# Kernel tuning notes

Measured on AMD Instinct MI355X. Metric: run time of the kernel, lower is better.

The kernel has to match this reference:

```python
import jax, jax.numpy as jnp
import numpy as np

B, T, E = 2, 4096, 1024
H = 16
D = E // H  # head_len = 64


def setup_inputs() -> dict:
    key = jax.random.key(0)
    ks = jax.random.split(key, 6)
    s = 1.0 / np.sqrt(E)
    return {
        "x": jax.random.normal(ks[0], (B, T, E), dtype=jnp.float32),
        # torch nn.Linear weights: shape (out, in), y = x @ W.T
        "Wq": jax.random.uniform(ks[1], (E, E), jnp.float32, -s, s),
        "Wk": jax.random.uniform(ks[2], (E, E), jnp.float32, -s, s),
        "Wv": jax.random.uniform(ks[3], (E, E), jnp.float32, -s, s),
        "Wo": jax.random.uniform(ks[4], (E, E), jnp.float32, -s, s),
        "bo": jax.random.uniform(ks[5], (E,), jnp.float32, -s, s),
    }


def reference(x, Wq, Wk, Wv, Wo, bo):
    Bx, Tx, Ex = x.shape
    q = x @ Wq.T
    k = x @ Wk.T
    v = x @ Wv.T
    # (B, T, H, D) -> (B, H, T, D)
    q = q.reshape(Bx, Tx, H, D).transpose(0, 2, 1, 3)
    k = k.reshape(Bx, Tx, H, D).transpose(0, 2, 1, 3)
    v = v.reshape(Bx, Tx, H, D).transpose(0, 2, 1, 3)
    # scores: (B, H, T, T), scaled by sqrt(head_len)
    sim = jnp.einsum("bhqd,bhkd->bhqk", q, k) / jnp.sqrt(jnp.float32(D))
    causal = jnp.tril(jnp.ones((Tx, Tx), dtype=bool))  # True = keep
    sim = jnp.where(causal[None, None], sim, -jnp.inf)
    attn = jax.nn.softmax(sim, axis=-1)
    # dropout_rate = 0.0 (eval) -> identity
    out = jnp.einsum("bhqk,bhkd->bhqd", attn, v)
    out = out.transpose(0, 2, 1, 3).reshape(Bx, Tx, Ex)
    return out @ Wo.T + bo
```

## Files before the change

kernel.cpp:

```cpp
#include <hip/hip_runtime.h>

typedef unsigned short bf16_t;
typedef __bf16 bf16x8 __attribute__((ext_vector_type(8)));
typedef float  v4f   __attribute__((ext_vector_type(4)));

__device__ __forceinline__ bf16_t f2bf(float f) {
    union { float f; unsigned u; } a; a.f = f;
    unsigned r = a.u + 0x7FFFu + ((a.u >> 16) & 1u);
    return (bf16_t)(r >> 16);
}
__device__ __forceinline__ unsigned fbits(float f) {
    union { float f; unsigned u; } a; a.f = f; return a.u;
}
__device__ __forceinline__ unsigned pk_trunc(float lo, float hi) {
    return (fbits(lo) >> 16) | (fbits(hi) & 0xFFFF0000u);
}

#define GL16(g, l) __builtin_amdgcn_global_load_lds( \
    (__attribute__((address_space(1))) void*)(g),    \
    (__attribute__((address_space(3))) void*)(l), 16, 0, 0)

#define QSCALE 0.18033688011f

__global__ __launch_bounds__(256) void cvt_all(
    const float4* __restrict__ x,  const float4* __restrict__ wq,
    const float4* __restrict__ wk, const float4* __restrict__ wv,
    const float4* __restrict__ wo,
    ushort4* __restrict__ xb, ushort4* __restrict__ wqkv, ushort4* __restrict__ wob) {
    int i = blockIdx.x * 256 + threadIdx.x;
    const float4* s; ushort4* d; int off;
    if (i < 2097152) { s = x; d = xb; off = i; }
    else {
        int wdx = (i - 2097152) >> 18;
        off = (i - 2097152) & 262143;
        if      (wdx == 0) { s = wq; d = wqkv; }
        else if (wdx == 1) { s = wk; d = wqkv + 262144; }
        else if (wdx == 2) { s = wv; d = wqkv + 524288; }
        else               { s = wo; d = wob; }
    }
    float4 v = s[off];
    ushort4 o;
    o.x = f2bf(v.x); o.y = f2bf(v.y); o.z = f2bf(v.z); o.w = f2bf(v.w);
    d[off] = o;
}

#define GEMM_MAINLOOP(A_, W_)                                                          \
    __shared__ bf16_t SMEM[8192];                                                      \
    bf16_t* As = SMEM; bf16_t* Bs = SMEM + 4096;                                       \
    const int tid = threadIdx.x;                                                       \
    const int w = tid >> 6, lane = tid & 63;                                           \
    const int lrow = lane & 15, lq = lane >> 4;                                        \
    const int m0 = blockIdx.y * 128, n0 = blockIdx.x * 128;                            \
    const int srow = w * 16 + (lane >> 2);                                             \
    const int sk = (lane & 3) * 8;                                                     \
    const int wm = (w & 1) * 64, wn = (w >> 1) * 64;                                   \
    v4f acc[4][4];                                                                     \
    _Pragma("unroll") for (int i = 0; i < 4; ++i)                                      \
        _Pragma("unroll") for (int j = 0; j < 4; ++j)                                  \
            acc[i][j] = (v4f){0.f, 0.f, 0.f, 0.f};                                     \
    for (int k0 = 0; k0 < 1024; k0 += 32) {                                            \
        __syncthreads();                                                               \
        GL16(A_ + (size_t)(m0 + srow) * 1024 + k0 + sk,      (char*)As + w * 1024);    \
        GL16(A_ + (size_t)(m0 + 64 + srow) * 1024 + k0 + sk, (char*)As + 4096 + w * 1024); \
        GL16(W_ + (size_t)(n0 + srow) * 1024 + k0 + sk,      (char*)Bs + w * 1024);    \
        GL16(W_ + (size_t)(n0 + 64 + srow) * 1024 + k0 + sk, (char*)Bs + 4096 + w * 1024); \
        __syncthreads();                                                               \
        bf16x8 af[4], bf[4];                                                           \
        _Pragma("unroll") for (int i = 0; i < 4; ++i)                                  \
            af[i] = *(const bf16x8*)&As[(wm + i * 16 + lrow) * 32 + lq * 8];           \
        _Pragma("unroll") for (int j = 0; j < 4; ++j)                                  \
            bf[j] = *(const bf16x8*)&Bs[(wn + j * 16 + lrow) * 32 + lq * 8];           \
        _Pragma("unroll") for (int i = 0; i < 4; ++i)                                  \
            _Pragma("unroll") for (int j = 0; j < 4; ++j)                              \
                acc[i][j] = __builtin_amdgcn_mfma_f32_16x16x32_bf16(af[i], bf[j],      \
                                                                    acc[i][j], 0, 0, 0); \
    }

__global__ __launch_bounds__(256) void gemm_qkv_kernel(
    const bf16_t* __restrict__ A, const bf16_t* __restrict__ W,
    bf16_t* __restrict__ Qb, bf16_t* __restrict__ Kb, bf16_t* __restrict__ Vtb) {
    GEMM_MAINLOOP(A, W)
    const int x = blockIdx.x;
    const int b = m0 >> 12, t0 = m0 & 4095;
    if (x < 8) {
#pragma unroll
        for (int i = 0; i < 4; ++i)
#pragma unroll
            for (int j = 0; j < 4; ++j)
#pragma unroll
                for (int r = 0; r < 4; ++r) {
                    int t = t0 + wm + i * 16 + lq * 4 + r;
                    int n = n0 + wn + j * 16 + lrow;
                    int h = n >> 6, d = n & 63;
                    Qb[(((size_t)b * 16 + h) * 4096 + t) * 64 + d] =
                        f2bf(acc[i][j][r] * QSCALE);
                }
    } else if (x < 16) {
#pragma unroll
        for (int i = 0; i < 4; ++i)
#pragma unroll
            for (int j = 0; j < 4; ++j)
#pragma unroll
                for (int r = 0; r < 4; ++r) {
                    int t = t0 + wm + i * 16 + lq * 4 + r;
                    int nn = n0 + wn + j * 16 + lrow - 1024;
                    int h = nn >> 6, d = nn & 63;
                    Kb[(((size_t)b * 16 + h) * 4096 + t) * 64 + d] = f2bf(acc[i][j][r]);
                }
    } else {
        const int d0 = n0 - 2048;
#pragma unroll 1
        for (int p = 0; p < 2; ++p) {
            __syncthreads();
            if ((w >> 1) == p) {
#pragma unroll
                for (int i = 0; i < 4; ++i)
#pragma unroll
                    for (int j = 0; j < 4; ++j) {
                        int row = j * 16 + lrow;
                        int swz = (row & 7) << 1;
                        int g = (wm >> 2) + i * 4 + lq;
                        uint2 u;
                        u.x = (unsigned)f2bf(acc[i][j][0]) | ((unsigned)f2bf(acc[i][j][1]) << 16);
                        u.y = (unsigned)f2bf(acc[i][j][2]) | ((unsigned)f2bf(acc[i][j][3]) << 16);
                        *(uint2*)&SMEM[row * 128 + ((g ^ swz) << 2)] = u;
                    }
            }
            __syncthreads();
#pragma unroll
            for (int uu = 0; uu < 4; ++uu) {
                int unit = tid + 256 * uu;
                int row = unit >> 4, seg = unit & 15;
                uint4 val = *(const uint4*)&SMEM[row * 128 + ((seg ^ (row & 7)) << 3)];
                *(uint4*)&Vtb[((size_t)b * 1024 + d0 + p * 64 + row) * 4096 + t0 + seg * 8] = val;
            }
        }
    }
}

__global__ __launch_bounds__(256) void gemm_out_kernel(
    const bf16_t* __restrict__ A, const bf16_t* __restrict__ W,
    const float* __restrict__ bo, float* __restrict__ out) {
    GEMM_MAINLOOP(A, W)
#pragma unroll
    for (int j = 0; j < 4; ++j) {
        int n = n0 + wn + j * 16 + lrow;
        float bias = bo[n];
#pragma unroll
        for (int i = 0; i < 4; ++i)
#pragma unroll
            for (int r = 0; r < 4; ++r) {
                int m = m0 + wm + i * 16 + lq * 4 + r;
                out[(size_t)m * 1024 + n] = acc[i][j][r] + bias;
            }
    }
}

__global__ __launch_bounds__(256, 2) void attn_kernel(
    const bf16_t* __restrict__ Q, const bf16_t* __restrict__ K,
    const bf16_t* __restrict__ Vt, bf16_t* __restrict__ O) {
    __shared__ bf16_t Kls[2][2][64 * 32];
    __shared__ bf16_t Vls[2][2][64 * 32];
    __shared__ bf16_t Plds[4][32 * 64];
    const int tid = threadIdx.x;
    const int w = tid >> 6, lane = tid & 63;
    const int lrow = lane & 15, lq = lane >> 4;
    const int bh = blockIdx.y;
    const int g = blockIdx.x;

    const bf16_t* Qh = Q + (size_t)bh * (4096 * 64);
    const bf16_t* Kh = K + (size_t)bh * (4096 * 64);
    const bf16_t* Vh = Vt + (size_t)bh * (64 * 4096);
    bf16_t* Pw = Plds[w];
    const int b = bh >> 4, h = bh & 15;

    const int srow = lane >> 2;
    const int soff = (((lane & 3) ^ (srow & 3))) * 8;
    const int kswz = (lq ^ (lrow & 3)) * 8;
    const int pswz = (lrow & 7) << 1;

    bf16x8 ones;
#pragma unroll
    for (int i = 0; i < 8; ++i) ones[i] = (__bf16)1.0f;

#pragma unroll 1
    for (int mem = 0; mem < 2; ++mem) {
        const int j = mem ? (31 - g) : g;
        const int q0 = j * 128;
        const int q0w = q0 + w * 32;
        const int nt = 2 * j + 2;
        const int wlast = 2 * j + (w >> 1);

        bf16x8 qf[2][2];
#pragma unroll
        for (int sub = 0; sub < 2; ++sub)
#pragma unroll
            for (int dk = 0; dk < 2; ++dk)
                qf[sub][dk] = *(const bf16x8*)&Qh[(size_t)(q0w + sub * 16 + lrow) * 64 + dk * 32 + lq * 8];

        v4f oacc[2][4];
        v4f lacc[2];
#pragma unroll
        for (int s2 = 0; s2 < 2; ++s2) {
            lacc[s2] = (v4f){0.f, 0.f, 0.f, 0.f};
#pragma unroll
            for (int d = 0; d < 4; ++d) oacc[s2][d] = (v4f){0.f, 0.f, 0.f, 0.f};
        }

        auto stage = [&](int kt, int buf) {
            const int kc0 = kt << 6;
#pragma unroll
            for (int i = 0; i < 2; ++i) {
                int idx = w * 2 + i;
                int half = idx >> 2, rg = idx & 3;
                GL16(Kh + (size_t)(kc0 + rg * 16 + srow) * 64 + half * 32 + soff,
                     (char*)&Kls[buf][half][rg * 512]);
                GL16(Vh + (size_t)(rg * 16 + srow) * 4096 + kc0 + half * 32 + soff,
                     (char*)&Vls[buf][half][rg * 512]);
            }
        };

        stage(0, 0);
        for (int kt = 0; kt < nt; ++kt) {
            const int buf = kt & 1;
            __syncthreads();
            if (kt + 1 < nt) stage(kt + 1, buf ^ 1);
            if (kt > wlast) continue;
            const int kc0 = kt << 6;
            const bool diag = (kt == wlast);

            bf16x8 kf0[4], kf1[4];
#pragma unroll
            for (int c = 0; c < 4; ++c) {
                kf0[c] = *(const bf16x8*)&Kls[buf][0][(c * 16 + lrow) * 32 + kswz];
                kf1[c] = *(const bf16x8*)&Kls[buf][1][(c * 16 + lrow) * 32 + kswz];
            }
            bf16x8 vf[4][2];
#pragma unroll
            for (int d = 0; d < 4; ++d)
#pragma unroll
                for (int kh = 0; kh < 2; ++kh)
                    vf[d][kh] = *(const bf16x8*)&Vls[buf][kh][(d * 16 + lrow) * 32 + kswz];

#pragma unroll
            for (int sub = 0; sub < 2; ++sub) {
                const int qrow = sub * 16 + lrow;
                const int qglob = q0w + qrow;

                v4f st[4];
#pragma unroll
                for (int c = 0; c < 4; ++c) {
                    v4f t0v = (v4f){0.f, 0.f, 0.f, 0.f};
                    t0v = __builtin_amdgcn_mfma_f32_16x16x32_bf16(kf0[c], qf[sub][0], t0v, 0, 0, 0);
                    st[c] = __builtin_amdgcn_mfma_f32_16x16x32_bf16(kf1[c], qf[sub][1], t0v, 0, 0, 0);
                }

#pragma unroll
                for (int c = 0; c < 4; ++c) {
                    float p[4];
#pragma unroll
                    for (int r = 0; r < 4; ++r) {
                        float pv = __builtin_amdgcn_exp2f(st[c][r]);
                        if (diag) {
                            int tg = kc0 + c * 16 + lq * 4 + r;
                            pv = (tg > qglob) ? 0.f : pv;
                        }
                        p[r] = pv;
                    }
                    uint2 u;
                    u.x = pk_trunc(p[0], p[1]);
                    u.y = pk_trunc(p[2], p[3]);
                    *(uint2*)&Pw[qrow * 64 + (((c * 4 + lq) ^ pswz) << 2)] = u;
                }

                bf16x8 pf[2];
#pragma unroll
                for (int kh = 0; kh < 2; ++kh) {
                    int s0 = kh * 8 + lq * 2;
                    pf[kh] = *(const bf16x8*)&Pw[qrow * 64 + ((s0 ^ pswz) << 2)];
                }

#pragma unroll
                for (int kh = 0; kh < 2; ++kh) {
                    lacc[sub] = __builtin_amdgcn_mfma_f32_16x16x32_bf16(pf[kh], ones, lacc[sub], 0, 0, 0);
#pragma unroll
                    for (int d = 0; d < 4; ++d)
                        oacc[sub][d] = __builtin_amdgcn_mfma_f32_16x16x32_bf16(pf[kh], vf[d][kh], oacc[sub][d], 0, 0, 0);
                }
            }
        }

#pragma unroll
        for (int sub = 0; sub < 2; ++sub) {
            float rl[4];
#pragma unroll
            for (int r = 0; r < 4; ++r) rl[r] = 1.0f / lacc[sub][r];
#pragma unroll
            for (int d = 0; d < 4; ++d)
#pragma unroll
                for (int r = 0; r < 4; ++r) {
                    int t = q0w + sub * 16 + lq * 4 + r;
                    O[((size_t)b * 4096 + t) * 1024 + h * 64 + d * 16 + lrow] =
                        f2bf(oacc[sub][d][r] * rl[r]);
                }
        }
    }
}

extern "C" void kernel_launch(void* const* d_in, const int* in_sizes, int n_in,
                              void* d_out, int out_size, void* d_ws, size_t ws_size,
                              hipStream_t stream) {
    const float* x  = (const float*)d_in[0];
    const float* Wq = (const float*)d_in[1];
    const float* Wk = (const float*)d_in[2];
    const float* Wv = (const float*)d_in[3];
    const float* Wo = (const float*)d_in[4];
    const float* bo = (const float*)d_in[5];
    float* out = (float*)d_out;

    char* ws = (char*)d_ws;
    bf16_t* xb   = (bf16_t*)(ws + 0);
    bf16_t* Wqkv = (bf16_t*)(ws + 16777216);
    bf16_t* Wob  = (bf16_t*)(ws + 23068672);
    bf16_t* Qb   = (bf16_t*)(ws + 25165824);
    bf16_t* Kb   = (bf16_t*)(ws + 41943040);
    bf16_t* Vtb  = (bf16_t*)(ws + 58720256);
    bf16_t* Ob   = (bf16_t*)(ws + 75497472);

    cvt_all<<<12288, 256, 0, stream>>>((const float4*)x, (const float4*)Wq,
                                       (const float4*)Wk, (const float4*)Wv,
                                       (const float4*)Wo,
                                       (ushort4*)xb, (ushort4*)Wqkv, (ushort4*)Wob);

    gemm_qkv_kernel<<<dim3(24, 64), 256, 0, stream>>>(xb, Wqkv, Qb, Kb, Vtb);

    attn_kernel<<<dim3(16, 32), 256, 0, stream>>>(Qb, Kb, Vtb, Ob);

    gemm_out_kernel<<<dim3(8, 64), 256, 0, stream>>>(Ob, Wob, bo, out);
}
```

Before: 314.2 us.

## Switch attention to 32x32 MFMA and keep P in registers via permlane swap

The attention inner loop moves from 16x16x32 to 32x32x16 bf16 MFMA tiles, with one 32-row query tile per wave instead of two 16-row sub-tiles. The P matrix no longer goes through LDS: the score layout is converted to the A-operand layout in registers using v_cvt_pk_bf16_f32 (round-to-nearest instead of truncation) and permlane32_swap. K/V staging now uses a single 64x64 XOR-swizzled LDS tile per buffer. This removes P LDS round-trips and the shared memory they used, and raises MFMA efficiency. The price is more accumulator registers per wave, which may limit occupancy.

```diff
diff --git a/kernel.cpp b/kernel.cpp
--- a/kernel.cpp
+++ b/kernel.cpp
@@ -3,17 +3,26 @@
 typedef unsigned short bf16_t;
 typedef __bf16 bf16x8 __attribute__((ext_vector_type(8)));
 typedef float  v4f   __attribute__((ext_vector_type(4)));
+typedef float  v16f  __attribute__((ext_vector_type(16)));
+typedef unsigned u32x2 __attribute__((ext_vector_type(2)));
 
 __device__ __forceinline__ bf16_t f2bf(float f) {
     union { float f; unsigned u; } a; a.f = f;
     unsigned r = a.u + 0x7FFFu + ((a.u >> 16) & 1u);
     return (bf16_t)(r >> 16);
 }
-__device__ __forceinline__ unsigned fbits(float f) {
-    union { float f; unsigned u; } a; a.f = f; return a.u;
-}
-__device__ __forceinline__ unsigned pk_trunc(float lo, float hi) {
-    return (fbits(lo) >> 16) | (fbits(hi) & 0xFFFF0000u);
+
+__device__ __forceinline__ unsigned cvtpk(float lo, float hi) {
+    unsigned r;
+    asm("v_cvt_pk_bf16_f32 %0, %1, %2" : "=v"(r) : "v"(lo), "v"(hi));
+    return r;
+}
+
+__device__ __forceinline__ v16f zero16() {
+    v16f z;
+#pragma unroll
+    for (int i = 0; i < 16; ++i) z[i] = 0.f;
+    return z;
 }
 
 #define GL16(g, l) __builtin_amdgcn_global_load_lds( \
@@ -159,25 +168,22 @@
 __global__ __launch_bounds__(256, 2) void attn_kernel(
     const bf16_t* __restrict__ Q, const bf16_t* __restrict__ K,
     const bf16_t* __restrict__ Vt, bf16_t* __restrict__ O) {
-    __shared__ bf16_t Kls[2][2][64 * 32];
-    __shared__ bf16_t Vls[2][2][64 * 32];
-    __shared__ bf16_t Plds[4][32 * 64];
+    __shared__ bf16_t Kls[2][64 * 64];
+    __shared__ bf16_t Vls[2][64 * 64];
     const int tid = threadIdx.x;
     const int w = tid >> 6, lane = tid & 63;
-    const int lrow = lane & 15, lq = lane >> 4;
+    const int l31 = lane & 31, lh = lane >> 5;
     const int bh = blockIdx.y;
     const int g = blockIdx.x;
 
     const bf16_t* Qh = Q + (size_t)bh * (4096 * 64);
     const bf16_t* Kh = K + (size_t)bh * (4096 * 64);
     const bf16_t* Vh = Vt + (size_t)bh * (64 * 4096);
-    bf16_t* Pw = Plds[w];
     const int b = bh >> 4, h = bh & 15;
 
-    const int srow = lane >> 2;
-    const int soff = (((lane & 3) ^ (srow & 3))) * 8;
-    const int kswz = (lq ^ (lrow & 3)) * 8;
-    const int pswz = (lrow & 7) << 1;
+    const int svrow = lane >> 3;
+    const int sg8 = ((lane & 7) ^ svrow) * 8;
+    const int rx = l31 & 7;
 
     bf16x8 ones;
 #pragma unroll
@@ -190,33 +196,22 @@
         const int q0w = q0 + w * 32;
         const int nt = 2 * j + 2;
         const int wlast = 2 * j + (w >> 1);
-
-        bf16x8 qf[2][2];
-#pragma unroll
-        for (int sub = 0; sub < 2; ++sub)
-#pragma unroll
-            for (int dk = 0; dk < 2; ++dk)
-                qf[sub][dk] = *(const bf16x8*)&Qh[(size_t)(q0w + sub * 16 + lrow) * 64 + dk * 32 + lq * 8];
-
-        v4f oacc[2][4];
-        v4f lacc[2];
-#pragma unroll
-        for (int s2 = 0; s2 < 2; ++s2) {
-            lacc[s2] = (v4f){0.f, 0.f, 0.f, 0.f};
-#pragma unroll
-            for (int d = 0; d < 4; ++d) oacc[s2][d] = (v4f){0.f, 0.f, 0.f, 0.f};
-        }
+        const int qglob = q0w + l31;
+
+        bf16x8 qf[4];
+#pragma unroll
+        for (int dk = 0; dk < 4; ++dk)
+            qf[dk] = *(const bf16x8*)&Qh[(size_t)(q0w + l31) * 64 + dk * 16 + lh * 8];
+
+        v16f oacc0 = zero16(), oacc1 = zero16(), lacc = zero16();
 
         auto stage = [&](int kt, int buf) {
             const int kc0 = kt << 6;
 #pragma unroll
             for (int i = 0; i < 2; ++i) {
-                int idx = w * 2 + i;
-                int half = idx >> 2, rg = idx & 3;
-                GL16(Kh + (size_t)(kc0 + rg * 16 + srow) * 64 + half * 32 + soff,
-                     (char*)&Kls[buf][half][rg * 512]);
-                GL16(Vh + (size_t)(rg * 16 + srow) * 4096 + kc0 + half * 32 + soff,
-                     (char*)&Vls[buf][half][rg * 512]);
+                int r0 = w * 16 + i * 8;
+                GL16(Kh + (size_t)(kc0 + r0 + svrow) * 64 + sg8, (char*)&Kls[buf][r0 * 64]);
+                GL16(Vh + (size_t)(r0 + svrow) * 4096 + kc0 + sg8, (char*)&Vls[buf][r0 * 64]);
             }
         };
 
@@ -229,80 +224,71 @@
             const int kc0 = kt << 6;
             const bool diag = (kt == wlast);
 
-            bf16x8 kf0[4], kf1[4];
-#pragma unroll
-            for (int c = 0; c < 4; ++c) {
-                kf0[c] = *(const bf16x8*)&Kls[buf][0][(c * 16 + lrow) * 32 + kswz];
-                kf1[c] = *(const bf16x8*)&Kls[buf][1][(c * 16 + lrow) * 32 + kswz];
-            }
-            bf16x8 vf[4][2];
-#pragma unroll
-            for (int d = 0; d < 4; ++d)
-#pragma unroll
-                for (int kh = 0; kh < 2; ++kh)
-                    vf[d][kh] = *(const bf16x8*)&Vls[buf][kh][(d * 16 + lrow) * 32 + kswz];
-
-#pragma unroll
-            for (int sub = 0; sub < 2; ++sub) {
-                const int qrow = sub * 16 + lrow;
-                const int qglob = q0w + qrow;
-
-                v4f st[4];
-#pragma unroll
-                for (int c = 0; c < 4; ++c) {
-                    v4f t0v = (v4f){0.f, 0.f, 0.f, 0.f};
-                    t0v = __builtin_amdgcn_mfma_f32_16x16x32_bf16(kf0[c], qf[sub][0], t0v, 0, 0, 0);
-                    st[c] = __builtin_amdgcn_mfma_f32_16x16x32_bf16(kf1[c], qf[sub][1], t0v, 0, 0, 0);
+            bf16x8 kf[2][4];
+#pragma unroll
+            for (int th = 0; th < 2; ++th)
+#pragma unroll
+                for (int dk = 0; dk < 4; ++dk)
+                    kf[th][dk] = *(const bf16x8*)
+                        &Kls[buf][(th * 32 + l31) * 64 + (((dk * 2 + lh) ^ rx) * 8)];
+            bf16x8 vf[2][4];
+#pragma unroll
+            for (int db = 0; db < 2; ++db)
+#pragma unroll
+                for (int kb = 0; kb < 4; ++kb)
+                    vf[db][kb] = *(const bf16x8*)
+                        &Vls[buf][(db * 32 + l31) * 64 + (((kb * 2 + lh) ^ rx) * 8)];
+
+            v16f st0 = zero16(), st1 = zero16();
+#pragma unroll
+            for (int dk = 0; dk < 4; ++dk) {
+                st0 = __builtin_amdgcn_mfma_f32_32x32x16_bf16(kf[0][dk], qf[dk], st0, 0, 0, 0);
+                st1 = __builtin_amdgcn_mfma_f32_32x32x16_bf16(kf[1][dk], qf[dk], st1, 0, 0, 0);
+            }
+
+            bf16x8 pa[4];
+#pragma unroll
+            for (int th = 0; th < 2; ++th) {
+                float p[16];
+#pragma unroll
+                for (int r = 0; r < 16; ++r) {
+                    float pv = __builtin_amdgcn_exp2f(th ? st1[r] : st0[r]);
+                    if (diag) {
+                        int tg = kc0 + th * 32 + (r & 3) + 8 * (r >> 2) + 4 * lh;
+                        pv = (tg > qglob) ? 0.f : pv;
+                    }
+                    p[r] = pv;
                 }
-
-#pragma unroll
-                for (int c = 0; c < 4; ++c) {
-                    float p[4];
-#pragma unroll
-                    for (int r = 0; r < 4; ++r) {
-                        float pv = __builtin_amdgcn_exp2f(st[c][r]);
-                        if (diag) {
-                            int tg = kc0 + c * 16 + lq * 4 + r;
-                            pv = (tg > qglob) ? 0.f : pv;
-                        }
-                        p[r] = pv;
-                    }
-                    uint2 u;
-                    u.x = pk_trunc(p[0], p[1]);
-                    u.y = pk_trunc(p[2], p[3]);
-                    *(uint2*)&Pw[qrow * 64 + (((c * 4 + lq) ^ pswz) << 2)] = u;
+#pragma unroll
+                for (int kb2 = 0; kb2 < 2; ++kb2) {
+                    unsigned x0 = cvtpk(p[kb2 * 8 + 0], p[kb2 * 8 + 1]);
+                    unsigned x1 = cvtpk(p[kb2 * 8 + 2], p[kb2 * 8 + 3]);
+                    unsigned y0 = cvtpk(p[kb2 * 8 + 4], p[kb2 * 8 + 5]);
+                    unsigned y1 = cvtpk(p[kb2 * 8 + 6], p[kb2 * 8 + 7]);
+                    u32x2 ra = __builtin_amdgcn_permlane32_swap(x0, y0, false, false);
+                    u32x2 rb = __builtin_amdgcn_permlane32_swap(x1, y1, false, false);
+                    union { unsigned u[4]; bf16x8 v; } pu;
+                    pu.u[0] = ra.x; pu.u[1] = rb.x;
+                    pu.u[2] = ra.y; pu.u[3] = rb.y;
+                    pa[th * 2 + kb2] = pu.v;
                 }
-
-                bf16x8 pf[2];
-#pragma unroll
-                for (int kh = 0; kh < 2; ++kh) {
-                    int s0 = kh * 8 + lq * 2;
-                    pf[kh] = *(const bf16x8*)&Pw[qrow * 64 + ((s0 ^ pswz) << 2)];
-                }
-
-#pragma unroll
-                for (int kh = 0; kh < 2; ++kh) {
-                    lacc[sub] = __builtin_amdgcn_mfma_f32_16x16x32_bf16(pf[kh], ones, lacc[sub], 0, 0, 0);
-#pragma unroll
-                    for (int d = 0; d < 4; ++d)
-                        oacc[sub][d] = __builtin_amdgcn_mfma_f32_16x16x32_bf16(pf[kh], vf[d][kh], oacc[sub][d], 0, 0, 0);
-                }
+            }
+
+#pragma unroll
+            for (int kb = 0; kb < 4; ++kb) {
+                lacc  = __builtin_amdgcn_mfma_f32_32x32x16_bf16(pa[kb], ones,       lacc,  0, 0, 0);
+                oacc0 = __builtin_amdgcn_mfma_f32_32x32x16_bf16(pa[kb], vf[0][kb], oacc0, 0, 0, 0);
+                oacc1 = __builtin_amdgcn_mfma_f32_32x32x16_bf16(pa[kb], vf[1][kb], oacc1, 0, 0, 0);
             }
         }
 
 #pragma unroll
-        for (int sub = 0; sub < 2; ++sub) {
-            float rl[4];
-#pragma unroll
-            for (int r = 0; r < 4; ++r) rl[r] = 1.0f / lacc[sub][r];
-#pragma unroll
-            for (int d = 0; d < 4; ++d)
-#pragma unroll
-                for (int r = 0; r < 4; ++r) {
-                    int t = q0w + sub * 16 + lq * 4 + r;
-                    O[((size_t)b * 4096 + t) * 1024 + h * 64 + d * 16 + lrow] =
-                        f2bf(oacc[sub][d][r] * rl[r]);
-                }
+        for (int r = 0; r < 16; ++r) {
+            float rl = 1.0f / lacc[r];
+            int q = q0w + (r & 3) + 8 * (r >> 2) + 4 * lh;
+            size_t o0 = ((size_t)b * 4096 + q) * 1024 + h * 64;
+            O[o0 + l31]      = f2bf(oacc0[r] * rl);
+            O[o0 + 32 + l31] = f2bf(oacc1[r] * rl);
         }
     }
 }
```

Result: faster. 304.3 us (-3.1%).
